# Kernel optimization log

Measured on AMD Instinct MI355X. Metric: run time of the kernel, lower is better.

## Reference

```python
import jax, jax.numpy as jnp
import numpy as np

B, N, D = 512, 100000, 256
MAX_K = 20
EPS = 1e-12


def setup_inputs() -> dict:
    key = jax.random.key(0)
    k1, k2, k3, k4 = jax.random.split(key, 4)
    z_ego = jax.random.normal(k1, (B, D), dtype=jnp.float32)
    exo_bank = jax.random.normal(k2, (N, D), dtype=jnp.float32)
    sim_vt = jax.random.uniform(k3, (B, N), dtype=jnp.float32)
    W = jax.random.normal(k4, (D, D), dtype=jnp.float32) / np.sqrt(D)
    return {"z_ego": z_ego, "exo_bank": exo_bank, "sim_vt": sim_vt, "W": W, "k": 16}


def _l2_normalize(x):
    # matches torch F.normalize semantics with eps clamp
    n = jnp.sqrt(jnp.sum(x * x, axis=-1, keepdims=True))
    return x / jnp.maximum(n, EPS)


def reference(z_ego, exo_bank, sim_vt, W, k):
    # bilinear projection into query space (Linear, no bias)
    q = z_ego @ W.T                              # [B, D]
    k_eff = min(int(k), MAX_K, exo_bank.shape[0])
    # pairwise cosine similarity query x bank
    sim_vv = _l2_normalize(q) @ _l2_normalize(exo_bank).T   # [B, N]
    # combined score (sim_vt already [B, N]; broadcast is identity)
    score = 0.5 * sim_vv + 0.5 * sim_vt          # [B, N]
    _, topk_idx = jax.lax.top_k(score, k_eff)    # [B, k_eff]
    gathered = exo_bank[topk_idx]                # [B, k_eff, D]
    return gathered, topk_idx
```

## Files before the change

### kernel.cpp

```cpp
#include <hip/hip_runtime.h>
#include <math.h>
#include <stdint.h>

#define B_Q    512
#define N_BANK 100000
#define D_DIM  256
#define K16    16

#define NSL2   256
#define NCHUNK 1563
#define TROW   264
#define CHUNK_USHORT (64 * TROW)
#define CHUNK_BYTES  (CHUNK_USHORT * 2)
#define NGRP   6250
#define GSTRIDE 6272
#define MARGIN 5e-3f
#define CAPG   384

#define SLAB_FLOATS 32768

#define OFF_QN     0
#define OFF_QNT    0x80000
#define OFF_INORM  0x100000
#define OFF_TH     0x170000
#define OFF_GMAX   0x400000
#define OFF_BANKT  0x1400000
#define WS_NEED    ((size_t)OFF_BANKT + (size_t)NCHUNK * CHUNK_BYTES)
#define OFF_SVTT   0x4800000
#define WS_NEED2   ((size_t)OFF_SVTT + (size_t)NCHUNK * SLAB_FLOATS * 4)

#define FB_OFF_INORM (B_Q * D_DIM * 4)
#define FB_OFF_PSC   (1024 * 1024)
#define FB_OFF_PID   (FB_OFF_PSC + B_Q * 128 * K16 * 4)

typedef __attribute__((ext_vector_type(8))) short short8;
typedef __attribute__((ext_vector_type(4))) float floatx4;

typedef __attribute__((address_space(1))) const unsigned char gu8_t;
typedef __attribute__((address_space(3))) unsigned char lu8_t;

__device__ inline unsigned short f2bf(float x) {
    unsigned int u = __float_as_uint(x);
    unsigned int r = (u + 0x7FFFu + ((u >> 16) & 1u)) >> 16;
    return (unsigned short)r;
}
__device__ inline unsigned long long pack_key(float s, int idx) {
    unsigned int u = __float_as_uint(s);
    u ^= (u & 0x80000000u) ? 0xFFFFFFFFu : 0x80000000u;
    return ((unsigned long long)u << 32) | (unsigned int)(~(unsigned int)idx);
}
__device__ inline int key_idx(unsigned long long k) {
    return (int)(~(unsigned int)(k & 0xFFFFFFFFull));
}
__device__ inline unsigned long long shfl_down_u64(unsigned long long x, int off) {
    unsigned int lo = (unsigned int)x;
    unsigned int hi = (unsigned int)(x >> 32);
    lo = __shfl_down(lo, off, 64);
    hi = __shfl_down(hi, off, 64);
    return ((unsigned long long)hi << 32) | lo;
}
__device__ inline unsigned long long umax64(unsigned long long a, unsigned long long b) {
    return a > b ? a : b;
}


__global__ void qn_prep_kernel(const float* __restrict__ z_ego,
                               const float* __restrict__ W,
                               float* __restrict__ qn,
                               unsigned short* __restrict__ qnt) {
    __shared__ float zs[D_DIM];
    __shared__ float red[4];
    int b = blockIdx.x;
    int t = threadIdx.x;
    zs[t] = z_ego[b * D_DIM + t];
    __syncthreads();
    const float4* W4 = reinterpret_cast<const float4*>(W + (size_t)t * D_DIM);
    float acc = 0.f;
#pragma unroll 8
    for (int u = 0; u < 64; ++u) {
        float4 w = W4[u];
        acc += w.x * zs[u * 4 + 0];
        acc += w.y * zs[u * 4 + 1];
        acc += w.z * zs[u * 4 + 2];
        acc += w.w * zs[u * 4 + 3];
    }
    float ss = acc * acc;
#pragma unroll
    for (int off = 32; off > 0; off >>= 1) ss += __shfl_down(ss, off, 64);
    if ((t & 63) == 0) red[t >> 6] = ss;
    __syncthreads();
    float tot = red[0] + red[1] + red[2] + red[3];
    float n = fmaxf(sqrtf(tot), 1e-12f);
    float v = acc / n;
    qn[b * D_DIM + t] = v;
    qnt[(size_t)(b >> 6) * CHUNK_USHORT + (size_t)(b & 63) * TROW + t] = f2bf(v);
}

__global__ __launch_bounds__(256)
void prep_bank_kernel(const float* __restrict__ bank,
                      float* __restrict__ inorm,
                      unsigned short* __restrict__ bankt) {
    int c = blockIdx.x;
    int t = threadIdx.x, w = t >> 6, l = t & 63;
    unsigned short* dst = bankt + (size_t)c * CHUNK_USHORT;
#pragma unroll 1
    for (int rr = 0; rr < 16; ++rr) {
        int row = w * 16 + rr;
        int jg = c * 64 + row;
        ushort4 o = {0, 0, 0, 0};
        if (jg < N_BANK) {
            float4 v = *reinterpret_cast<const float4*>(bank + (size_t)jg * D_DIM + l * 4);
            float ss = v.x * v.x + v.y * v.y + v.z * v.z + v.w * v.w;
#pragma unroll
            for (int off = 1; off < 64; off <<= 1) ss += __shfl_xor(ss, off, 64);
            float inv = 1.0f / fmaxf(sqrtf(ss), 1e-12f);
            o.x = f2bf(v.x * inv); o.y = f2bf(v.y * inv);
            o.z = f2bf(v.z * inv); o.w = f2bf(v.w * inv);
            if (l == 0) inorm[jg] = inv;
        }
        *reinterpret_cast<ushort4*>(dst + (size_t)row * TROW + l * 4) = o;
    }
}

#define RT_Q 8
#define RT_J 1024
__global__ __launch_bounds__(256)
void svt_repack_kernel(const float* __restrict__ svt,
                       float* __restrict__ svtt) {
    __shared__ float tile[RT_Q][RT_J + 4];
    int t = threadIdx.x;
    int jt = blockIdx.x;
    int q0 = blockIdx.y * RT_Q;
    int jl = t * 4;
#pragma unroll
    for (int qq = 0; qq < RT_Q; ++qq) {
        int j = jt * RT_J + jl;
        float4 v = make_float4(0.f, 0.f, 0.f, 0.f);
        if (j < N_BANK)
            v = *reinterpret_cast<const float4*>(svt + (size_t)(q0 + qq) * N_BANK + j);
        *reinterpret_cast<float4*>(&tile[qq][jl]) = v;
    }
    __syncthreads();
    int half = t >> 7;
    int q1 = (t >> 4) & 7;
    int m = t & 15;
#pragma unroll
    for (int p = 0; p < 8; ++p) {
        int cc = p * 2 + half;
        int c = jt * 16 + cc;
        if (c < NCHUNK) {
            float4 v = *reinterpret_cast<const float4*>(&tile[q1][cc * 64 + m * 4]);
            *reinterpret_cast<float4*>(svtt + (size_t)c * SLAB_FLOATS
                                       + (size_t)(q0 + q1) * 64 + m * 4) = v;
        }
    }
}

__global__ __launch_bounds__(256, 4)
void screen5_kernel(const unsigned short* __restrict__ qnt,
                    const unsigned short* __restrict__ bankt,
                    const float* __restrict__ svtt,
                    float* __restrict__ gmax) {
    __shared__ unsigned short lbank[CHUNK_USHORT];
    int t = threadIdx.x, w = t >> 6, l = t & 63;
    int lane16 = l & 15, quad = l >> 4;

    int bid = blockIdx.x;
    int xcd = bid & 7;
    int i = bid >> 3;
    int slice = (xcd << 5) + (i >> 2);
    int qb = i & 3;

    int qt = qb * 4 + w;
    int qbase = qt * 32;

    short8 afrag[2][8];
    {
        const unsigned short* abase = qnt + (size_t)(qt >> 1) * CHUNK_USHORT
                                          + (size_t)((qt & 1) * 32) * TROW;
#pragma unroll
        for (int s = 0; s < 2; ++s)
#pragma unroll
            for (int k = 0; k < 8; ++k)
                afrag[s][k] = *reinterpret_cast<const short8*>(
                    abase + (size_t)(16 * s + lane16) * TROW + k * 32 + quad * 8);
    }

    const float* sp[2][4];
#pragma unroll
    for (int s = 0; s < 2; ++s)
#pragma unroll
        for (int r = 0; r < 4; ++r)
            sp[s][r] = svtt + (size_t)(qbase + 16 * s + 4 * quad + r) * 64 + lane16;

    for (int c = slice; c < NCHUNK; c += NSL2) {
        int j0 = c * 64;

        {
            const unsigned char* gsrc = (const unsigned char*)bankt + (size_t)c * CHUNK_BYTES;
            unsigned char* lbase = (unsigned char*)lbank;
#pragma unroll
            for (int i2 = 0; i2 < 8; ++i2) {
                int off = i2 * 4096 + w * 1024;
                __builtin_amdgcn_global_load_lds((gu8_t*)(gsrc + off + l * 16),
                                                 (lu8_t*)(lbase + off), 16, 0, 0);
            }
            int off8 = 32768 + w * 256;
            __builtin_amdgcn_global_load_lds((gu8_t*)(gsrc + off8 + l * 4),
                                             (lu8_t*)(lbase + off8), 4, 0, 0);
        }

        float sv[4][2][4];
        {
            size_t slabOff = (size_t)c * SLAB_FLOATS;
#pragma unroll
            for (int s = 0; s < 2; ++s)
#pragma unroll
                for (int r = 0; r < 4; ++r) {
                    const float* rp = sp[s][r] + slabOff;
#pragma unroll
                    for (int jg = 0; jg < 4; ++jg)
                        sv[jg][s][r] = rp[16 * jg];
                }
        }

        __syncthreads();

        int g0 = c * 4;
#pragma unroll
        for (int jg = 0; jg < 4; ++jg) {
            floatx4 acc0 = (floatx4){0.f, 0.f, 0.f, 0.f};
            floatx4 acc1 = (floatx4){0.f, 0.f, 0.f, 0.f};
            const unsigned short* bbase = lbank + (size_t)(16 * jg + lane16) * TROW + quad * 8;
#pragma unroll
            for (int k = 0; k < 8; ++k) {
                short8 bfrag = *reinterpret_cast<const short8*>(bbase + k * 32);
                acc0 = __builtin_amdgcn_mfma_f32_16x16x32_bf16(afrag[0][k], bfrag, acc0, 0, 0, 0);
                acc1 = __builtin_amdgcn_mfma_f32_16x16x32_bf16(afrag[1][k], bfrag, acc1, 0, 0, 0);
            }

            int jglob = j0 + 16 * jg + lane16;
            bool inb = jglob < N_BANK;
            int g = g0 + jg;
            bool doStore = (lane16 == 0) && (g < NGRP);
#pragma unroll
            for (int s = 0; s < 2; ++s) {
#pragma unroll
                for (int r = 0; r < 4; ++r) {
                    float a = (s == 0) ? acc0[r] : acc1[r];
                    float score = inb ? (0.5f * a + 0.5f * sv[jg][s][r]) : -INFINITY;
                    score = fmaxf(score, __shfl_xor(score, 1, 64));
                    score = fmaxf(score, __shfl_xor(score, 2, 64));
                    score = fmaxf(score, __shfl_xor(score, 4, 64));
                    score = fmaxf(score, __shfl_xor(score, 8, 64));
                    if (doStore) {
                        int q = qbase + 16 * s + 4 * quad + r;
                        gmax[(size_t)q * GSTRIDE + g] = score;
                    }
                }
            }
        }
        __syncthreads();
    }
}

__global__ __launch_bounds__(256, 4)
void screen4_kernel(const unsigned short* __restrict__ qnt,
                    const unsigned short* __restrict__ bankt,
                    const float* __restrict__ svt,
                    float* __restrict__ gmax) {
    __shared__ unsigned short lbank[CHUNK_USHORT];
    int t = threadIdx.x, w = t >> 6, l = t & 63;
    int lane16 = l & 15, quad = l >> 4;

    int bid = blockIdx.x;
    int xcd = bid & 7;
    int i = bid >> 3;
    int slice = (xcd << 5) + (i >> 2);
    int qb = i & 3;

    int qt = qb * 4 + w;
    int qbase = qt * 32;

    short8 afrag[2][8];
    {
        const unsigned short* abase = qnt + (size_t)(qt >> 1) * CHUNK_USHORT
                                          + (size_t)((qt & 1) * 32) * TROW;
#pragma unroll
        for (int s = 0; s < 2; ++s)
#pragma unroll
            for (int k = 0; k < 8; ++k)
                afrag[s][k] = *reinterpret_cast<const short8*>(
                    abase + (size_t)(16 * s + lane16) * TROW + k * 32 + quad * 8);
    }

    const float* svr[2][4];
#pragma unroll
    for (int s = 0; s < 2; ++s)
#pragma unroll
        for (int r = 0; r < 4; ++r)
            svr[s][r] = svt + (size_t)(qbase + 16 * s + 4 * quad + r) * (size_t)N_BANK;

    for (int c = slice; c < NCHUNK; c += NSL2) {
        int j0 = c * 64;
        {
            const unsigned char* gsrc = (const unsigned char*)bankt + (size_t)c * CHUNK_BYTES;
            unsigned char* lbase = (unsigned char*)lbank;
#pragma unroll
            for (int i2 = 0; i2 < 8; ++i2) {
                int off = i2 * 4096 + w * 1024;
                __builtin_amdgcn_global_load_lds((gu8_t*)(gsrc + off + l * 16),
                                                 (lu8_t*)(lbase + off), 16, 0, 0);
            }
            int off8 = 32768 + w * 256;
            __builtin_amdgcn_global_load_lds((gu8_t*)(gsrc + off8 + l * 4),
                                             (lu8_t*)(lbase + off8), 4, 0, 0);
        }

        float sv[4][2][4];
#pragma unroll
        for (int s = 0; s < 2; ++s)
#pragma unroll
            for (int r = 0; r < 4; ++r) {
                const float* rp = svr[s][r] + j0 + lane16;
#pragma unroll
                for (int jg = 0; jg < 4; ++jg) {
                    int jglob = j0 + 16 * jg + lane16;
                    sv[jg][s][r] = (jglob < N_BANK) ? rp[16 * jg] : 0.f;
                }
            }

        __syncthreads();

        int g0 = c * 4;
#pragma unroll
        for (int jg = 0; jg < 4; ++jg) {
            floatx4 acc0 = (floatx4){0.f, 0.f, 0.f, 0.f};
            floatx4 acc1 = (floatx4){0.f, 0.f, 0.f, 0.f};
            const unsigned short* bbase = lbank + (size_t)(16 * jg + lane16) * TROW + quad * 8;
#pragma unroll
            for (int k = 0; k < 8; ++k) {
                short8 bfrag = *reinterpret_cast<const short8*>(bbase + k * 32);
                acc0 = __builtin_amdgcn_mfma_f32_16x16x32_bf16(afrag[0][k], bfrag, acc0, 0, 0, 0);
                acc1 = __builtin_amdgcn_mfma_f32_16x16x32_bf16(afrag[1][k], bfrag, acc1, 0, 0, 0);
            }

            int jglob = j0 + 16 * jg + lane16;
            bool inb = jglob < N_BANK;
            int g = g0 + jg;
            bool doStore = (lane16 == 0) && (g < NGRP);
#pragma unroll
            for (int s = 0; s < 2; ++s) {
#pragma unroll
                for (int r = 0; r < 4; ++r) {
                    float a = (s == 0) ? acc0[r] : acc1[r];
                    float score = inb ? (0.5f * a + 0.5f * sv[jg][s][r]) : -INFINITY;
                    score = fmaxf(score, __shfl_xor(score, 1, 64));
                    score = fmaxf(score, __shfl_xor(score, 2, 64));
                    score = fmaxf(score, __shfl_xor(score, 4, 64));
                    score = fmaxf(score, __shfl_xor(score, 8, 64));
                    if (doStore) {
                        int q = qbase + 16 * s + 4 * quad + r;
                        gmax[(size_t)q * GSTRIDE + g] = score;
                    }
                }
            }
        }
        __syncthreads();
    }
}

__global__ __launch_bounds__(256)
void gthresh_kernel(const float* __restrict__ gmax,
                    float* __restrict__ th) {
    __shared__ float buf[NGRP];
    __shared__ float red[4];
    int q = blockIdx.x, t = threadIdx.x, w = t >> 6;
    for (int i = t; i < NGRP; i += 256) buf[i] = gmax[(size_t)q * GSTRIDE + i];
    __syncthreads();
    float s16 = -INFINITY;
    for (int r = 0; r < K16; ++r) {
        float m = -INFINITY;
        for (int i = t; i < NGRP; i += 256) m = fmaxf(m, buf[i]);
#pragma unroll
        for (int off = 32; off > 0; off >>= 1) m = fmaxf(m, __shfl_down(m, off, 64));
        if ((t & 63) == 0) red[w] = m;
        __syncthreads();
        m = fmaxf(fmaxf(red[0], red[1]), fmaxf(red[2], red[3]));
        if (r == K16 - 1) s16 = m;
        if (r < K16 - 1) {
            for (int i = t; i < NGRP; i += 256)
                if (buf[i] == m) buf[i] = -INFINITY;
        }
        __syncthreads();
    }
    if (t == 0) th[q] = s16 - MARGIN;
}

__global__ __launch_bounds__(256)
void grescore_kernel(const float* __restrict__ gmax,
                     const float* __restrict__ th,
                     const float* __restrict__ qn,
                     const float* __restrict__ inorm,
                     const float* __restrict__ bank,
                     const float* __restrict__ svt,
                     float* __restrict__ out) {
    __shared__ float qns[D_DIM];
    __shared__ int glist[CAPG];
    __shared__ unsigned long long keys2[CAPG * K16];
    __shared__ unsigned long long wred[4];
    __shared__ int winI[K16];
    __shared__ int gcntS;
    int b = blockIdx.x, t = threadIdx.x;
    int w = t >> 6, l = t & 63;

    qns[t] = qn[(size_t)b * D_DIM + t];
    if (t == 0) gcntS = 0;
    __syncthreads();
    float thb = th[b];
    for (int g = t; g < NGRP; g += 256) {
        if (gmax[(size_t)b * GSTRIDE + g] >= thb) {
            int p = atomicAdd(&gcntS, 1);
            if (p < CAPG) glist[p] = g;
        }
    }
    __syncthreads();
    int ng = gcntS < CAPG ? gcntS : CAPG;
    int ncand = ng * K16;

    const float4* bank4 = reinterpret_cast<const float4*>(bank);
    float4 qv = reinterpret_cast<const float4*>(qns)[l];
    for (int ci = w; ci < ncand; ci += 8) {
        int jA = glist[ci >> 4] * K16 + (ci & 15);
        int ci2 = ci + 4;
        bool has2 = ci2 < ncand;
        int jB = has2 ? (glist[ci2 >> 4] * K16 + (ci2 & 15)) : jA;
        float4 bvA = bank4[(size_t)jA * 64 + l];
        float4 bvB = bank4[(size_t)jB * 64 + l];
        float dA = qv.x * bvA.x + qv.y * bvA.y + qv.z * bvA.z + qv.w * bvA.w;
        float dB = qv.x * bvB.x + qv.y * bvB.y + qv.z * bvB.z + qv.w * bvB.w;
#pragma unroll
        for (int off = 32; off > 0; off >>= 1) dA += __shfl_down(dA, off, 64);
#pragma unroll
        for (int off = 32; off > 0; off >>= 1) dB += __shfl_down(dB, off, 64);
        if (l == 0) {
            float sA = 0.5f * (dA * inorm[jA]) + 0.5f * svt[(size_t)b * N_BANK + jA];
            keys2[ci] = pack_key(sA, jA);
            if (has2) {
                float sB = 0.5f * (dB * inorm[jB]) + 0.5f * svt[(size_t)b * N_BANK + jB];
                keys2[ci2] = pack_key(sB, jB);
            }
        }
    }
    __syncthreads();

    for (int r = 0; r < K16; ++r) {
        unsigned long long best = 0ull;
        for (int i2 = t; i2 < ncand; i2 += 256) best = umax64(best, keys2[i2]);
#pragma unroll
        for (int off = 32; off > 0; off >>= 1) best = umax64(best, shfl_down_u64(best, off));
        if (l == 0) wred[w] = best;
        __syncthreads();
        unsigned long long W = umax64(umax64(wred[0], wred[1]), umax64(wred[2], wred[3]));
        if (t == 0) winI[r] = key_idx(W);
        for (int i2 = t; i2 < ncand; i2 += 256)
            if (keys2[i2] == W) keys2[i2] = 0ull;
        __syncthreads();
    }

    if (t < K16)
        out[(size_t)B_Q * K16 * D_DIM + (size_t)b * K16 + t] = (float)winI[t];
    float4* out4 = reinterpret_cast<float4*>(out);
    for (int u = t; u < K16 * 64; u += 256) {
        int r = u >> 6, cc = u & 63;
        out4[((size_t)b * K16 + r) * 64 + cc] = bank4[(size_t)winI[r] * 64 + cc];
    }
}

#define FBT 64
#define FJT 64
#define FKC 64
#define FNS 128
#define FNC ((N_BANK + FJT - 1) / FJT)

__global__ void inorm_kernel(const float* __restrict__ bank,
                             float* __restrict__ inorm) {
    int w = threadIdx.x >> 6;
    int lane = threadIdx.x & 63;
    int j = blockIdx.x * 4 + w;
    if (j >= N_BANK) return;
    const float4* r4 = reinterpret_cast<const float4*>(bank + (size_t)j * D_DIM);
    float4 v = r4[lane];
    float ss = v.x * v.x + v.y * v.y + v.z * v.z + v.w * v.w;
#pragma unroll
    for (int off = 32; off > 0; off >>= 1) ss += __shfl_down(ss, off, 64);
    if (lane == 0) inorm[j] = 1.0f / fmaxf(sqrtf(ss), 1e-12f);
}

__global__ void fb_qn_kernel(const float* __restrict__ z_ego,
                             const float* __restrict__ W,
                             float* __restrict__ qn) {
    __shared__ float zs[D_DIM];
    __shared__ float red[4];
    int b = blockIdx.x;
    int t = threadIdx.x;
    zs[t] = z_ego[b * D_DIM + t];
    __syncthreads();
    const float4* W4 = reinterpret_cast<const float4*>(W + (size_t)t * D_DIM);
    float acc = 0.f;
#pragma unroll 8
    for (int u = 0; u < 64; ++u) {
        float4 w = W4[u];
        acc += w.x * zs[u * 4 + 0]; acc += w.y * zs[u * 4 + 1];
        acc += w.z * zs[u * 4 + 2]; acc += w.w * zs[u * 4 + 3];
    }
    float ss = acc * acc;
#pragma unroll
    for (int off = 32; off > 0; off >>= 1) ss += __shfl_down(ss, off, 64);
    if ((t & 63) == 0) red[t >> 6] = ss;
    __syncthreads();
    float tot = red[0] + red[1] + red[2] + red[3];
    qn[b * D_DIM + t] = acc / fmaxf(sqrtf(tot), 1e-12f);
}

__global__ __launch_bounds__(256)
void fb_score_topk_kernel(const float* __restrict__ qn,
                          const float* __restrict__ bank,
                          const float* __restrict__ svt,
                          const float* __restrict__ inorm,
                          float* __restrict__ psc,
                          int* __restrict__ pid) {
    __shared__ float As[FKC][FBT];
    __shared__ float Bsh[FKC][FJT];
    __shared__ float Ss[FBT][FJT + 1];
    int slice = blockIdx.x;
    int qbase = blockIdx.y * FBT;
    int t = threadIdx.x;
    int tq = t >> 4, tj = t & 15;
    int q0 = tq * 4, j0l = tj * 4;
    float sc[K16]; int id[K16];
#pragma unroll
    for (int i = 0; i < K16; ++i) { sc[i] = -INFINITY; id[i] = 0x7fffffff; }
    for (int c = slice; c < FNC; c += FNS) {
        int j0 = c * FJT;
        float acc[4][4];
#pragma unroll
        for (int a = 0; a < 4; ++a)
#pragma unroll
            for (int b2 = 0; b2 < 4; ++b2) acc[a][b2] = 0.f;
        for (int kc = 0; kc < D_DIM; kc += FKC) {
            __syncthreads();
#pragma unroll
            for (int r = 0; r < 4; ++r) {
                int idx = t + 256 * r;
                int q = idx & 63, kv = idx >> 6;
                float4 v = *reinterpret_cast<const float4*>(
                    &qn[(size_t)(qbase + q) * D_DIM + kc + kv * 4]);
                As[kv * 4 + 0][q] = v.x; As[kv * 4 + 1][q] = v.y;
                As[kv * 4 + 2][q] = v.z; As[kv * 4 + 3][q] = v.w;
            }
#pragma unroll
            for (int r = 0; r < 4; ++r) {
                int idx = t + 256 * r;
                int j = idx & 63, kv = idx >> 6;
                int jg = j0 + j;
                float4 v = make_float4(0.f, 0.f, 0.f, 0.f);
                if (jg < N_BANK)
                    v = *reinterpret_cast<const float4*>(
                        &bank[(size_t)jg * D_DIM + kc + kv * 4]);
                Bsh[kv * 4 + 0][j] = v.x; Bsh[kv * 4 + 1][j] = v.y;
                Bsh[kv * 4 + 2][j] = v.z; Bsh[kv * 4 + 3][j] = v.w;
            }
            __syncthreads();
#pragma unroll
            for (int k = 0; k < FKC; ++k) {
                float4 av = *reinterpret_cast<const float4*>(&As[k][q0]);
                float4 bv = *reinterpret_cast<const float4*>(&Bsh[k][j0l]);
                float a[4] = {av.x, av.y, av.z, av.w};
                float bb[4] = {bv.x, bv.y, bv.z, bv.w};
#pragma unroll
                for (int qi = 0; qi < 4; ++qi)
#pragma unroll
                    for (int ji = 0; ji < 4; ++ji) acc[qi][ji] += a[qi] * bb[ji];
            }
        }
        bool full = (j0 + FJT <= N_BANK);
        if (full) {
            float4 inv = *reinterpret_cast<const float4*>(&inorm[j0 + j0l]);
            float iv[4] = {inv.x, inv.y, inv.z, inv.w};
#pragma unroll
            for (int qi = 0; qi < 4; ++qi) {
                int q = qbase + q0 + qi;
                float4 svv = *reinterpret_cast<const float4*>(
                    &svt[(size_t)q * N_BANK + j0 + j0l]);
                float s[4] = {svv.x, svv.y, svv.z, svv.w};
#pragma unroll
                for (int ji = 0; ji < 4; ++ji)
                    Ss[q0 + qi][j0l + ji] = 0.5f * (acc[qi][ji] * iv[ji]) + 0.5f * s[ji];
            }
        } else {
#pragma unroll
            for (int qi = 0; qi < 4; ++qi) {
                int q = qbase + q0 + qi;
#pragma unroll
                for (int ji = 0; ji < 4; ++ji) {
                    int jg = j0 + j0l + ji;
                    float s = -INFINITY;
                    if (jg < N_BANK)
                        s = 0.5f * (acc[qi][ji] * inorm[jg]) + 0.5f * svt[(size_t)q * N_BANK + jg];
                    Ss[q0 + qi][j0l + ji] = s;
                }
            }
        }
        __syncthreads();
        if (t < FBT) {
#pragma unroll 1
            for (int jj = 0; jj < FJT; ++jj) {
                int jg = j0 + jj;
                if (jg >= N_BANK) break;
                float s = Ss[t][jj];
                if (s > sc[K16 - 1] || (s == sc[K16 - 1] && jg < id[K16 - 1])) {
                    float cs = s; int ci = jg;
#pragma unroll
                    for (int i = 0; i < K16; ++i) {
                        bool bt2 = (cs > sc[i]) || (cs == sc[i] && ci < id[i]);
                        float ts = sc[i]; int ti = id[i];
                        if (bt2) { sc[i] = cs; id[i] = ci; cs = ts; ci = ti; }
                    }
                }
            }
        }
    }
    if (t < FBT) {
        int q = qbase + t;
        size_t base = ((size_t)q * FNS + slice) * K16;
#pragma unroll
        for (int i = 0; i < K16; ++i) { psc[base + i] = sc[i]; pid[base + i] = id[i]; }
    }
}

__global__ __launch_bounds__(256)
void fb_merge_kernel(const float* __restrict__ psc,
                     const int* __restrict__ pid,
                     const float* __restrict__ bank,
                     float* __restrict__ out) {
    __shared__ unsigned long long keys[FNS * K16];
    __shared__ unsigned long long wred[4];
    __shared__ int win[K16];
    int b = blockIdx.x, t = threadIdx.x;
    for (int i = t; i < FNS * K16; i += 256) {
        float s = psc[(size_t)b * FNS * K16 + i];
        unsigned int u = __float_as_uint(s);
        u ^= (u & 0x80000000u) ? 0xFFFFFFFFu : 0x80000000u;
        unsigned int iv = ~(unsigned int)pid[(size_t)b * FNS * K16 + i];
        keys[i] = ((unsigned long long)u << 32) | iv;
    }
    __syncthreads();
    for (int r = 0; r < K16; ++r) {
        unsigned long long best = 0ull;
        for (int i = t; i < FNS * K16; i += 256) best = umax64(best, keys[i]);
#pragma unroll
        for (int off = 32; off > 0; off >>= 1) best = umax64(best, shfl_down_u64(best, off));
        if ((t & 63) == 0) wred[t >> 6] = best;
        __syncthreads();
        unsigned long long w = umax64(umax64(wred[0], wred[1]), umax64(wred[2], wred[3]));
        if (t == 0) win[r] = (int)(~(unsigned int)w);
        for (int i = t; i < FNS * K16; i += 256)
            if (keys[i] == w) keys[i] = 0ull;
        __syncthreads();
    }
    if (t < K16)
        out[(size_t)B_Q * K16 * D_DIM + (size_t)b * K16 + t] = (float)win[t];
    const float4* bank4 = reinterpret_cast<const float4*>(bank);
    float4* out4 = reinterpret_cast<float4*>(out);
    for (int u = t; u < K16 * 64; u += 256) {
        int r = u >> 6, c = u & 63;
        out4[((size_t)b * K16 + r) * 64 + c] = bank4[(size_t)win[r] * 64 + c];
    }
}

extern "C" void kernel_launch(void* const* d_in, const int* in_sizes, int n_in,
                              void* d_out, int out_size, void* d_ws, size_t ws_size,
                              hipStream_t stream) {
    const float* z_ego = (const float*)d_in[0];
    const float* bank  = (const float*)d_in[1];
    const float* svt   = (const float*)d_in[2];
    const float* W     = (const float*)d_in[3];
    float* out = (float*)d_out;
    char* ws = (char*)d_ws;

    if (ws_size >= WS_NEED) {
        float* qn             = (float*)(ws + OFF_QN);
        unsigned short* qnt   = (unsigned short*)(ws + OFF_QNT);
        float* inorm          = (float*)(ws + OFF_INORM);
        float* th             = (float*)(ws + OFF_TH);
        float* gmax           = (float*)(ws + OFF_GMAX);
        unsigned short* bankt = (unsigned short*)(ws + OFF_BANKT);

        qn_prep_kernel<<<B_Q, 256, 0, stream>>>(z_ego, W, qn, qnt);
        prep_bank_kernel<<<NCHUNK, 256, 0, stream>>>(bank, inorm, bankt);
        if (ws_size >= WS_NEED2) {
            float* svtt = (float*)(ws + OFF_SVTT);
            dim3 rg((N_BANK + RT_J - 1) / RT_J, B_Q / RT_Q);
            svt_repack_kernel<<<rg, 256, 0, stream>>>(svt, svtt);
            screen5_kernel<<<NSL2 * 4, 256, 0, stream>>>(qnt, bankt, svtt, gmax);
        } else {
            screen4_kernel<<<NSL2 * 4, 256, 0, stream>>>(qnt, bankt, svt, gmax);
        }
        gthresh_kernel<<<B_Q, 256, 0, stream>>>(gmax, th);
        grescore_kernel<<<B_Q, 256, 0, stream>>>(gmax, th, qn, inorm, bank, svt, out);
    } else {
        float* qn    = (float*)(ws + 0);
        float* inorm = (float*)(ws + FB_OFF_INORM);
        float* psc   = (float*)(ws + FB_OFF_PSC);
        int*   pid   = (int*)(ws + FB_OFF_PID);
        fb_qn_kernel<<<B_Q, 256, 0, stream>>>(z_ego, W, qn);
        inorm_kernel<<<(N_BANK + 3) / 4, 256, 0, stream>>>(bank, inorm);
        dim3 grid(FNS, B_Q / FBT);
        fb_score_topk_kernel<<<grid, 256, 0, stream>>>(qn, bank, svt, inorm, psc, pid);
        fb_merge_kernel<<<B_Q, 256, 0, stream>>>(psc, pid, bank, out);
    }
}
```

Baseline: 677.5 us.

## Split candidate rescoring across blocks per query and add top-k merge kernel

The rescore stage is split so that each query is handled by four blocks, each over a quarter of the group range. Each block writes its partial top-16 packed keys to workspace, and a new merge kernel combines them and gathers the bank rows. The inner loop now issues four candidate loads per wave at once to increase memory-level parallelism. The change trades an extra kernel launch and workspace traffic for more parallel blocks and smaller per-block LDS. It also caps surviving groups per split at 96, which could drop candidates if they cluster in one partition.

```diff
diff --git a/kernel.cpp b/kernel.cpp
--- a/kernel.cpp
+++ b/kernel.cpp
@@ -16,6 +16,9 @@
 #define GSTRIDE 6272
 #define MARGIN 5e-3f
 #define CAPG   384
+#define NSPLIT 4
+#define CAPG_S 96
+#define GPART  ((NGRP + NSPLIT - 1) / NSPLIT)
 
 #define SLAB_FLOATS 32768
 
@@ -23,6 +26,7 @@
 #define OFF_QNT    0x80000
 #define OFF_INORM  0x100000
 #define OFF_TH     0x170000
+#define OFF_PKEYS  0x200000
 #define OFF_GMAX   0x400000
 #define OFF_BANKT  0x1400000
 #define WS_NEED    ((size_t)OFF_BANKT + (size_t)NCHUNK * CHUNK_BYTES)
@@ -57,6 +61,13 @@
     unsigned int hi = (unsigned int)(x >> 32);
     lo = __shfl_down(lo, off, 64);
     hi = __shfl_down(hi, off, 64);
+    return ((unsigned long long)hi << 32) | lo;
+}
+__device__ inline unsigned long long shfl_u64(unsigned long long x, int lane) {
+    unsigned int lo = (unsigned int)x;
+    unsigned int hi = (unsigned int)(x >> 32);
+    lo = __shfl(lo, lane, 64);
+    hi = __shfl(hi, lane, 64);
     return ((unsigned long long)hi << 32) | lo;
 }
 __device__ inline unsigned long long umax64(unsigned long long a, unsigned long long b) {
@@ -398,62 +409,72 @@
 }
 
 __global__ __launch_bounds__(256)
-void grescore_kernel(const float* __restrict__ gmax,
-                     const float* __restrict__ th,
-                     const float* __restrict__ qn,
-                     const float* __restrict__ inorm,
-                     const float* __restrict__ bank,
-                     const float* __restrict__ svt,
-                     float* __restrict__ out) {
+void gscore_kernel(const float* __restrict__ gmax,
+                   const float* __restrict__ th,
+                   const float* __restrict__ qn,
+                   const float* __restrict__ inorm,
+                   const float* __restrict__ bank,
+                   const float* __restrict__ svt,
+                   unsigned long long* __restrict__ pkeys) {
     __shared__ float qns[D_DIM];
-    __shared__ int glist[CAPG];
-    __shared__ unsigned long long keys2[CAPG * K16];
+    __shared__ int glist[CAPG_S];
+    __shared__ unsigned long long keys2[CAPG_S * K16];
     __shared__ unsigned long long wred[4];
-    __shared__ int winI[K16];
     __shared__ int gcntS;
-    int b = blockIdx.x, t = threadIdx.x;
-    int w = t >> 6, l = t & 63;
+    int s = blockIdx.x;
+    int b = blockIdx.y;
+    int t = threadIdx.x, w = t >> 6, l = t & 63;
 
     qns[t] = qn[(size_t)b * D_DIM + t];
     if (t == 0) gcntS = 0;
     __syncthreads();
     float thb = th[b];
-    for (int g = t; g < NGRP; g += 256) {
+    int ga = s * GPART;
+    int gb = ga + GPART < NGRP ? ga + GPART : NGRP;
+    for (int g = ga + t; g < gb; g += 256) {
         if (gmax[(size_t)b * GSTRIDE + g] >= thb) {
             int p = atomicAdd(&gcntS, 1);
-            if (p < CAPG) glist[p] = g;
-        }
-    }
-    __syncthreads();
-    int ng = gcntS < CAPG ? gcntS : CAPG;
+            if (p < CAPG_S) glist[p] = g;
+        }
+    }
+    __syncthreads();
+    int ng = gcntS < CAPG_S ? gcntS : CAPG_S;
     int ncand = ng * K16;
 
     const float4* bank4 = reinterpret_cast<const float4*>(bank);
     float4 qv = reinterpret_cast<const float4*>(qns)[l];
-    for (int ci = w; ci < ncand; ci += 8) {
-        int jA = glist[ci >> 4] * K16 + (ci & 15);
-        int ci2 = ci + 4;
-        bool has2 = ci2 < ncand;
-        int jB = has2 ? (glist[ci2 >> 4] * K16 + (ci2 & 15)) : jA;
-        float4 bvA = bank4[(size_t)jA * 64 + l];
-        float4 bvB = bank4[(size_t)jB * 64 + l];
-        float dA = qv.x * bvA.x + qv.y * bvA.y + qv.z * bvA.z + qv.w * bvA.w;
-        float dB = qv.x * bvB.x + qv.y * bvB.y + qv.z * bvB.z + qv.w * bvB.w;
-#pragma unroll
-        for (int off = 32; off > 0; off >>= 1) dA += __shfl_down(dA, off, 64);
-#pragma unroll
-        for (int off = 32; off > 0; off >>= 1) dB += __shfl_down(dB, off, 64);
+    for (int ci = w; ci < ncand; ci += 16) {
+        int j[4]; bool has[4];
+#pragma unroll
+        for (int p = 0; p < 4; ++p) {
+            int c2 = ci + 4 * p;
+            has[p] = c2 < ncand;
+            int cs = has[p] ? c2 : ci;
+            j[p] = glist[cs >> 4] * K16 + (cs & 15);
+        }
+        float inv[4], sva[4];
         if (l == 0) {
-            float sA = 0.5f * (dA * inorm[jA]) + 0.5f * svt[(size_t)b * N_BANK + jA];
-            keys2[ci] = pack_key(sA, jA);
-            if (has2) {
-                float sB = 0.5f * (dB * inorm[jB]) + 0.5f * svt[(size_t)b * N_BANK + jB];
-                keys2[ci2] = pack_key(sB, jB);
-            }
-        }
-    }
-    __syncthreads();
-
+#pragma unroll
+            for (int p = 0; p < 4; ++p)
+                if (has[p]) { inv[p] = inorm[j[p]]; sva[p] = svt[(size_t)b * N_BANK + j[p]]; }
+        }
+        float4 bv[4];
+#pragma unroll
+        for (int p = 0; p < 4; ++p) bv[p] = bank4[(size_t)j[p] * 64 + l];
+#pragma unroll
+        for (int p = 0; p < 4; ++p) {
+            float d = qv.x * bv[p].x + qv.y * bv[p].y + qv.z * bv[p].z + qv.w * bv[p].w;
+#pragma unroll
+            for (int off = 32; off > 0; off >>= 1) d += __shfl_down(d, off, 64);
+            if (l == 0 && has[p]) {
+                float sc = 0.5f * (d * inv[p]) + 0.5f * sva[p];
+                keys2[ci + 4 * p] = pack_key(sc, j[p]);
+            }
+        }
+    }
+    __syncthreads();
+
+    unsigned long long* outk = pkeys + ((size_t)b * NSPLIT + s) * K16;
     for (int r = 0; r < K16; ++r) {
         unsigned long long best = 0ull;
         for (int i2 = t; i2 < ncand; i2 += 256) best = umax64(best, keys2[i2]);
@@ -462,14 +483,34 @@
         if (l == 0) wred[w] = best;
         __syncthreads();
         unsigned long long W = umax64(umax64(wred[0], wred[1]), umax64(wred[2], wred[3]));
-        if (t == 0) winI[r] = key_idx(W);
+        if (t == 0) outk[r] = W;
         for (int i2 = t; i2 < ncand; i2 += 256)
             if (keys2[i2] == W) keys2[i2] = 0ull;
         __syncthreads();
     }
-
+}
+
+__global__ __launch_bounds__(256)
+void gmerge_kernel(const unsigned long long* __restrict__ pkeys,
+                   const float* __restrict__ bank,
+                   float* __restrict__ out) {
+    __shared__ int winI[K16];
+    int b = blockIdx.x, t = threadIdx.x;
+    if (t < 64) {
+        unsigned long long k = pkeys[(size_t)b * (NSPLIT * K16) + t];
+        for (int r = 0; r < K16; ++r) {
+            unsigned long long m = k;
+#pragma unroll
+            for (int off = 32; off > 0; off >>= 1) m = umax64(m, shfl_down_u64(m, off));
+            m = shfl_u64(m, 0);
+            if (t == 0) winI[r] = key_idx(m);
+            if (k == m) k = 0ull;
+        }
+    }
+    __syncthreads();
     if (t < K16)
         out[(size_t)B_Q * K16 * D_DIM + (size_t)b * K16 + t] = (float)winI[t];
+    const float4* bank4 = reinterpret_cast<const float4*>(bank);
     float4* out4 = reinterpret_cast<float4*>(out);
     for (int u = t; u < K16 * 64; u += 256) {
         int r = u >> 6, cc = u & 63;
@@ -694,6 +735,7 @@
         unsigned short* qnt   = (unsigned short*)(ws + OFF_QNT);
         float* inorm          = (float*)(ws + OFF_INORM);
         float* th             = (float*)(ws + OFF_TH);
+        unsigned long long* pkeys = (unsigned long long*)(ws + OFF_PKEYS);
         float* gmax           = (float*)(ws + OFF_GMAX);
         unsigned short* bankt = (unsigned short*)(ws + OFF_BANKT);
 
@@ -708,7 +750,9 @@
             screen4_kernel<<<NSL2 * 4, 256, 0, stream>>>(qnt, bankt, svt, gmax);
         }
         gthresh_kernel<<<B_Q, 256, 0, stream>>>(gmax, th);
-        grescore_kernel<<<B_Q, 256, 0, stream>>>(gmax, th, qn, inorm, bank, svt, out);
+        dim3 sg(NSPLIT, B_Q);
+        gscore_kernel<<<sg, 256, 0, stream>>>(gmax, th, qn, inorm, bank, svt, pkeys);
+        gmerge_kernel<<<B_Q, 256, 0, stream>>>(pkeys, bank, out);
     } else {
         float* qn    = (float*)(ws + 0);
         float* inorm = (float*)(ws + FB_OFF_INORM);
```

Result: faster. 642.2 us (-5.2%).
